# Kernel optimization log

Hardware: AMD Instinct MI355X
Metric: run time of the kernel (lower is better)

The kernel has to match this reference:

```python
import jax, jax.numpy as jnp
import numpy as np

HID = 256
STYLE_DIM = 64
NUM_STYLES = 8
IN_DIM = 3 + STYLE_DIM


def setup_inputs() -> dict:
    key = jax.random.key(0)
    ks = jax.random.split(key, 12)
    B, H, W = 2, 512, 512
    rgb = jax.random.uniform(ks[0], (B, 3, H, W), dtype=jnp.float32)
    style_idx = jax.random.randint(ks[1], (B,), 0, NUM_STYLES, dtype=jnp.int32)
    # style embedding table (torch init: normal std=0.01)
    emb_table = 0.01 * jax.random.normal(ks[2], (NUM_STYLES, STYLE_DIM), dtype=jnp.float32)
    # kaiming-normal (fan_in, relu gain sqrt(2)) weights stored as [in, out]
    def kaiming(k, fan_in, fan_out):
        std = np.sqrt(2.0 / fan_in)
        return std * jax.random.normal(k, (fan_in, fan_out), dtype=jnp.float32)
    W0 = kaiming(ks[3], IN_DIM, HID); b0 = jnp.zeros((HID,), jnp.float32)
    W1 = kaiming(ks[4], HID, HID);    b1 = jnp.zeros((HID,), jnp.float32)
    W2 = kaiming(ks[5], HID, HID);    b2 = jnp.zeros((HID,), jnp.float32)
    W3 = kaiming(ks[6], HID, 3);      b3 = jnp.zeros((3,), jnp.float32)
    return {"rgb": rgb, "style_idx": style_idx, "emb_table": emb_table,
            "W0": W0, "b0": b0, "W1": W1, "b1": b1,
            "W2": W2, "b2": b2, "W3": W3, "b3": b3}


def reference(rgb, style_idx, emb_table, W0, b0, W1, b1, W2, b2, W3, b3):
    B, C, H, W_ = rgb.shape  # CHW image input
    # [B,3,H,W] -> [B*H*W, 3]
    rgb_flat = jnp.transpose(rgb, (0, 2, 3, 1)).reshape(-1, 3)
    # style embedding lookup, broadcast per pixel
    emb = emb_table[style_idx]                              # [B, style_dim]
    emb = jnp.broadcast_to(emb[:, None, :], (B, H * W_, STYLE_DIM)).reshape(-1, STYLE_DIM)
    x = jnp.concatenate([rgb_flat, emb], axis=-1)           # [N, 67]
    gelu = lambda t: jax.nn.gelu(t, approximate=False)      # torch nn.GELU default (erf)
    x = gelu(x @ W0 + b0)
    x = gelu(x @ W1 + b1)
    x = gelu(x @ W2 + b2)
    out_flat = jax.nn.sigmoid(x @ W3 + b3)                  # [N, 3]
    out = out_flat.reshape(B, H, W_, 3).transpose(0, 3, 1, 2)
    return out
```

## Files before the change

### kernel.cpp

```cpp
#include <hip/hip_runtime.h>

#define HW  (512*512)

typedef _Float16 half8  __attribute__((__vector_size__(16)));
typedef float    floatx4 __attribute__((__vector_size__(16)));

__device__ __forceinline__ float gelu_f(float x){
    float x2 = x * x;
    float q  = __builtin_fmaf(x2, -0.1029432f, -2.3022079f);
    float e  = __builtin_amdgcn_exp2f(x * q);
    return x * __builtin_amdgcn_rcpf(1.0f + e);
}

__device__ __forceinline__ float sigmoid_f(float x){
    float e = __builtin_amdgcn_exp2f(-1.44269504f * x);
    return __builtin_amdgcn_rcpf(1.0f + e);
}

__device__ __forceinline__ int swz(int row){
    return ((row & 3) << 3) ^ (((row >> 2) & 3) << 4);
}

__global__ void prep_all(const float* __restrict__ W1, const float* __restrict__ W2,
                         const float* __restrict__ W3, const float* __restrict__ emb,
                         const int* __restrict__ sidx, const float* __restrict__ W0,
                         const float* __restrict__ b0,
                         _Float16* __restrict__ wp, float* __restrict__ c0){
    int blk = blockIdx.x;
    int tid = threadIdx.x;
    if (blk < 528){
        int gid = blk * 256 + tid;
        if (gid < 131072){
            int i    = gid & 65535;
            int j    = i & 7;
            int lane = (i >> 3) & 63;
            int b2   = i >> 9;
            int ks = b2 >> 4, nt = b2 & 15;
            int k = ks*32 + ((lane >> 4) << 3) + j;
            int n = nt*16 + (lane & 15);
            const float* W = (gid < 65536) ? W1 : W2;
            wp[gid] = (_Float16)W[k*256 + n];
        } else {
            int i    = gid - 131072;
            int j    = i & 7;
            int lane = (i >> 3) & 63;
            int ks   = i >> 9;
            int k = ks*32 + ((lane >> 4) << 3) + j;
            int n = lane & 15;
            wp[gid] = (_Float16)((n < 3) ? W3[k*3 + n] : 0.0f);
        }
    } else {
        int b = blk - 528;
        int s = sidx[b];
        float acc = b0[tid];
        #pragma unroll 8
        for (int d = 0; d < 64; d++)
            acc = fmaf(emb[s*64 + d], W0[(3 + d)*256 + tid], acc);
        c0[b*256 + tid] = acc;
    }
}

__global__ __launch_bounds__(512, 4)
void nilut_main(const float* __restrict__ rgb,
                const float* __restrict__ W0,
                const float* __restrict__ b1v,
                const float* __restrict__ b2v,
                const float* __restrict__ b3v,
                const _Float16* __restrict__ wp,
                const float* __restrict__ c0,
                float* __restrict__ out){
    __shared__ __align__(16) _Float16 act[128 * 256];
    __shared__ __align__(16) float    w0s[1024];
    __shared__ __align__(16) float    rgbs[384];

    const int tid = threadIdx.x;
    const int wg  = blockIdx.x;
    const int pixbase = wg * 128;
    const int b   = pixbase >> 18;
    const int hw0 = pixbase & (HW - 1);

    #pragma unroll
    for (int r = 0; r < 2; r++){
        int q = r*512 + tid;
        w0s[q] = (q < 768) ? W0[q] : c0[b*256 + (q - 768)];
    }
    if (tid < 384){
        int c = tid >> 7, row = tid & 127;
        rgbs[tid] = rgb[b*3*HW + c*HW + hw0 + row];
    }
    __syncthreads();

    {
        int ng = tid & 31;
        int rg = tid >> 5;
        floatx4 cw[4][2];
        #pragma unroll
        for (int p = 0; p < 4; p++){
            cw[p][0] = *(const floatx4*)&w0s[p*256 + ng*8];
            cw[p][1] = *(const floatx4*)&w0s[p*256 + ng*8 + 4];
        }
        #pragma unroll
        for (int hf = 0; hf < 2; hf++){
            floatx4 rv[3];
            #pragma unroll
            for (int c = 0; c < 3; c++)
                rv[c] = *(const floatx4*)&rgbs[c*128 + rg*8 + hf*4];
            #pragma unroll
            for (int r4 = 0; r4 < 4; r4++){
                int row = rg*8 + hf*4 + r4;
                float rr = rv[0][r4], gg = rv[1][r4], bb = rv[2][r4];
                half8 v;
                #pragma unroll
                for (int j = 0; j < 8; j++){
                    int hi = j >> 2, lo = j & 3;
                    float z = fmaf(rr, cw[0][hi][lo],
                              fmaf(gg, cw[1][hi][lo],
                              fmaf(bb, cw[2][hi][lo], cw[3][hi][lo])));
                    v[j] = (_Float16)gelu_f(z);
                }
                *(half8*)&act[row*256 + ((ng*8) ^ swz(row))] = v;
            }
        }
    }
    __syncthreads();

    const int lane = tid & 63;
    const int wv   = tid >> 6;
    const int ln15 = lane & 15;
    const int quad = lane >> 4;
    const int q8   = quad * 8;
    const int qr   = quad * 4;
    const int sA   = swz(ln15);

    const _Float16* wl  = wp;
    const float* bias   = b1v;
    const int mh = wv >> 2, nh = wv & 3;
    const int rbase = mh * 64;
    const int cb16  = nh * 4;
    #pragma unroll 1
    for (int L = 0; L < 2; L++){
        floatx4 acc[4][4];
        #pragma unroll
        for (int nt = 0; nt < 4; nt++){
            float bv = bias[(cb16 + nt)*16 + ln15];
            #pragma unroll
            for (int m = 0; m < 4; m++)
                acc[m][nt] = (floatx4){bv, bv, bv, bv};
        }

        const half8* wp8 = (const half8*)wl;
        #pragma unroll 2
        for (int ks = 0; ks < 8; ks++){
            int k0 = (ks*32 + q8) ^ sA;
            half8 a[4];
            #pragma unroll
            for (int m = 0; m < 4; m++)
                a[m] = *(const half8*)&act[(rbase + m*16 + ln15)*256 + k0];
            #pragma unroll
            for (int nt = 0; nt < 4; nt++){
                half8 bf = wp8[(ks*16 + cb16 + nt)*64 + lane];
                #pragma unroll
                for (int m = 0; m < 4; m++)
                    acc[m][nt] = __builtin_amdgcn_mfma_f32_16x16x32_f16(a[m], bf, acc[m][nt], 0, 0, 0);
            }
        }
        __syncthreads();
        #pragma unroll
        for (int nt = 0; nt < 4; nt++){
            int n = (cb16 + nt)*16 + ln15;
            #pragma unroll
            for (int m = 0; m < 4; m++){
                #pragma unroll
                for (int r = 0; r < 4; r++){
                    int row = rbase + m*16 + qr + r;
                    int se  = (r << 3) ^ (quad << 4);
                    act[row*256 + (n ^ se)] = (_Float16)gelu_f(acc[m][nt][r]);
                }
            }
        }
        __syncthreads();
        wl = wp + 65536;
        bias = b2v;
    }

    {
        const half8* wp8 = (const half8*)(wp + 131072);
        int rbf = wv * 16;
        floatx4 ac = (floatx4){0.f,0.f,0.f,0.f};
        #pragma unroll
        for (int ks = 0; ks < 8; ks++){
            int k0 = (ks*32 + q8) ^ sA;
            half8 a  = *(const half8*)&act[(rbf + ln15)*256 + k0];
            half8 bf = wp8[ks*64 + lane];
            ac = __builtin_amdgcn_mfma_f32_16x16x32_f16(a, bf, ac, 0, 0, 0);
        }
        if (ln15 < 3){
            float bv = b3v[ln15];
            #pragma unroll
            for (int r = 0; r < 4; r++){
                int row0 = rbf + qr + r;
                w0s[ln15*128 + row0] = sigmoid_f(ac[r] + bv);
            }
        }
        __syncthreads();
        if (tid < 96){
            int c  = tid >> 5;
            int i2 = tid & 31;
            float4* dst = (float4*)(out + (b*3 + c)*HW + hw0);
            dst[i2] = ((float4*)(w0s + c*128))[i2];
        }
    }
}

extern "C" void kernel_launch(void* const* d_in, const int* in_sizes, int n_in,
                              void* d_out, int out_size, void* d_ws, size_t ws_size,
                              hipStream_t stream){
    const float* rgb = (const float*)d_in[0];
    const int*  sidx = (const int*) d_in[1];
    const float* emb = (const float*)d_in[2];
    const float* W0  = (const float*)d_in[3];
    const float* b0  = (const float*)d_in[4];
    const float* W1  = (const float*)d_in[5];
    const float* b1  = (const float*)d_in[6];
    const float* W2  = (const float*)d_in[7];
    const float* b2  = (const float*)d_in[8];
    const float* W3  = (const float*)d_in[9];
    const float* b3  = (const float*)d_in[10];
    float* out = (float*)d_out;

    _Float16* wp = (_Float16*)d_ws;
    float*    c0 = (float*)((char*)d_ws + 270336);

    int n_pix = in_sizes[0] / 3;
    prep_all<<<530, 256, 0, stream>>>(W1, W2, W3, emb, sidx, W0, b0, wp, c0);
    nilut_main<<<n_pix / 128, 512, 0, stream>>>(rgb, W0, b1, b2, b3, wp, c0, out);
}
```

Measured before the change: 285.7 us.

## Simplify LDS swizzle, precompute epilogue offsets, tile weight packing through shared memory

Drops the row-low-bits term from the activation LDS swizzle, so the per-element epilogue store address becomes a precomputed base plus constant offsets, cutting integer address math. The weight prep kernel now packs W1/W2 through a shared-memory tile with coalesced vector loads and 16-byte stores, using 82 blocks instead of 530. The weaker swizzle may bring back LDS bank conflicts on the MFMA A-operand reads and the scattered fp16 epilogue stores.

```diff
diff --git a/kernel.cpp b/kernel.cpp
--- a/kernel.cpp
+++ b/kernel.cpp
@@ -18,7 +18,7 @@
 }
 
 __device__ __forceinline__ int swz(int row){
-    return ((row & 3) << 3) ^ (((row >> 2) & 3) << 4);
+    return ((row >> 2) & 3) << 4;
 }
 
 __global__ void prep_all(const float* __restrict__ W1, const float* __restrict__ W2,
@@ -26,31 +26,39 @@
                          const int* __restrict__ sidx, const float* __restrict__ W0,
                          const float* __restrict__ b0,
                          _Float16* __restrict__ wp, float* __restrict__ c0){
+    __shared__ float ld[32][68];
     int blk = blockIdx.x;
     int tid = threadIdx.x;
-    if (blk < 528){
-        int gid = blk * 256 + tid;
-        if (gid < 131072){
-            int i    = gid & 65535;
-            int j    = i & 7;
-            int lane = (i >> 3) & 63;
-            int b2   = i >> 9;
-            int ks = b2 >> 4, nt = b2 & 15;
-            int k = ks*32 + ((lane >> 4) << 3) + j;
-            int n = nt*16 + (lane & 15);
-            const float* W = (gid < 65536) ? W1 : W2;
-            wp[gid] = (_Float16)W[k*256 + n];
-        } else {
-            int i    = gid - 131072;
-            int j    = i & 7;
-            int lane = (i >> 3) & 63;
-            int ks   = i >> 9;
-            int k = ks*32 + ((lane >> 4) << 3) + j;
-            int n = lane & 15;
-            wp[gid] = (_Float16)((n < 3) ? W3[k*3 + n] : 0.0f);
-        }
+    if (blk < 64){
+        int mat = blk >> 5;
+        int g   = blk & 31;
+        int ks  = g >> 2;
+        int ntq = g & 3;
+        const float* W = mat ? W2 : W1;
+        int row = tid >> 3;
+        int c8  = (tid & 7) * 8;
+        const float* src = &W[(ks*32 + row)*256 + ntq*64 + c8];
+        *(floatx4*)&ld[row][c8]     = *(const floatx4*)src;
+        *(floatx4*)&ld[row][c8 + 4] = *(const floatx4*)(src + 4);
+        __syncthreads();
+        int lane = tid & 63;
+        int nt_l = tid >> 6;
+        half8 h;
+        #pragma unroll
+        for (int j = 0; j < 8; j++)
+            h[j] = (_Float16)ld[(lane >> 4)*8 + j][nt_l*16 + (lane & 15)];
+        _Float16* dst = wp + mat*65536 + (ks*16 + ntq*4 + nt_l)*512 + lane*8;
+        *(half8*)dst = h;
+    } else if (blk < 80){
+        int i    = (blk - 64)*256 + tid;
+        int j    = i & 7;
+        int lane = (i >> 3) & 63;
+        int ks   = i >> 9;
+        int k = ks*32 + ((lane >> 4) << 3) + j;
+        int n = lane & 15;
+        wp[131072 + i] = (_Float16)((n < 3) ? W3[k*3 + n] : 0.0f);
     } else {
-        int b = blk - 528;
+        int b = blk - 80;
         int s = sidx[b];
         float acc = b0[tid];
         #pragma unroll 8
@@ -137,6 +145,12 @@
     const int mh = wv >> 2, nh = wv & 3;
     const int rbase = mh * 64;
     const int cb16  = nh * 4;
+
+    int ebase[4];
+    #pragma unroll
+    for (int nt = 0; nt < 4; nt++)
+        ebase[nt] = (rbase + qr)*256 + (((cb16 + nt)*16 + ln15) ^ (quad << 4));
+
     #pragma unroll 1
     for (int L = 0; L < 2; L++){
         floatx4 acc[4][4];
@@ -167,15 +181,11 @@
         __syncthreads();
         #pragma unroll
         for (int nt = 0; nt < 4; nt++){
-            int n = (cb16 + nt)*16 + ln15;
             #pragma unroll
             for (int m = 0; m < 4; m++){
                 #pragma unroll
-                for (int r = 0; r < 4; r++){
-                    int row = rbase + m*16 + qr + r;
-                    int se  = (r << 3) ^ (quad << 4);
-                    act[row*256 + (n ^ se)] = (_Float16)gelu_f(acc[m][nt][r]);
-                }
+                for (int r = 0; r < 4; r++)
+                    act[ebase[nt] + m*4096 + r*256] = (_Float16)gelu_f(acc[m][nt][r]);
             }
         }
         __syncthreads();
@@ -232,6 +242,6 @@
     float*    c0 = (float*)((char*)d_ws + 270336);
 
     int n_pix = in_sizes[0] / 3;
-    prep_all<<<530, 256, 0, stream>>>(W1, W2, W3, emb, sidx, W0, b0, wp, c0);
+    prep_all<<<82, 256, 0, stream>>>(W1, W2, W3, emb, sidx, W0, b0, wp, c0);
     nilut_main<<<n_pix / 128, 512, 0, stream>>>(rgb, W0, b1, b2, b3, wp, c0, out);
 }
```

Measured after the change: 276.2 us. -3.3%, faster.
